# Optimization experiments

Hardware: AMD Instinct MI355X
Metric: run time of the kernel (lower is better)

Reference implementation:

```python
import jax, jax.numpy as jnp
import numpy as np

B, T, IN, H, BN, OUT = 512, 257, 32, 128, 256, 64
K_SUB = 4  # RK4 substeps per knot interval (fixed-step stand-in for adaptive cdeint)


def setup_inputs() -> dict:
    key = jax.random.key(0)
    ks = jax.random.split(key, 12)

    def gl(k, shape):
        fan_in = shape[0]
        return (jax.random.normal(k, shape, jnp.float32) / np.sqrt(fan_in)).astype(jnp.float32)

    t = jnp.arange(T, dtype=jnp.float32) * 0.05  # sorted time knots, t[0]=t0
    z0 = jax.random.normal(ks[0], (B, H), jnp.float32)
    # control path: smooth-ish random walk sampled at the knots
    X = jnp.cumsum(jax.random.normal(ks[1], (B, T, IN), jnp.float32) * 0.1, axis=1)
    return {
        "t": t, "z0": z0, "X": X,
        "W1": gl(ks[2], (H, BN)), "b1": jnp.zeros((BN,), jnp.float32),
        "W2": gl(ks[3], (BN, BN)), "b2": jnp.zeros((BN,), jnp.float32),
        "W3": gl(ks[4], (BN, IN * H)), "b3": jnp.zeros((IN * H,), jnp.float32),
        "mW": gl(ks[5], (H, OUT)), "mb": jnp.zeros((OUT,), jnp.float32),
        "sW": gl(ks[6], (H, OUT)), "sb": jnp.zeros((OUT,), jnp.float32),
    }


def reference(t, z0, X, W1, b1, W2, b2, W3, b3, mW, mb, sW, sb):
    def cde_func(z):  # z: [B,H] -> [B,H,IN]
        h = jax.nn.relu(z @ W1 + b1)
        h = jax.nn.relu(h @ W2 + b2)
        o = jnp.tanh(h @ W3 + b3)
        return o.reshape(z.shape[0], H, IN)

    def vf(z, dxdt):  # dz/dt = f(z) @ dX/dt
        return jnp.einsum('bhi,bi->bh', cde_func(z), dxdt)

    dt_int = t[1:] - t[:-1]                       # [T-1]
    dXdt = (X[:, 1:] - X[:, :-1]) / dt_int[None, :, None]  # [B,T-1,IN], const per interval

    def interval_step(z, inp):
        dxdt, dti = inp
        hstep = dti / K_SUB
        def sub(zc, _):
            k1 = vf(zc, dxdt)
            k2 = vf(zc + 0.5 * hstep * k1, dxdt)
            k3 = vf(zc + 0.5 * hstep * k2, dxdt)
            k4 = vf(zc + hstep * k3, dxdt)
            zn = zc + (hstep / 6.0) * (k1 + 2.0 * k2 + 2.0 * k3 + k4)
            return zn, None
        z, _ = jax.lax.scan(sub, z, None, length=K_SUB)
        return z, z

    _, zs = jax.lax.scan(interval_step, z0, (jnp.moveaxis(dXdt, 1, 0), dt_int))
    zs = jnp.moveaxis(zs, 0, 1)  # z at t[1:] -> [B, T-1, H] (matches [1:].permute(1,0,2))

    mean_pred = zs @ mW + mb
    std_pred = jax.nn.softplus(zs @ sW + sb)
    return mean_pred, std_pred
```

## Files before the change

kernel.cpp:

```cpp
#include <hip/hip_runtime.h>


using short8   = __attribute__((ext_vector_type(8))) short;
using float4v  = __attribute__((ext_vector_type(4))) float;

__device__ unsigned short g_w1p[32768];
__device__ unsigned short g_w2p[65536];
__device__ unsigned short g_w3p[1048576];
__device__ unsigned short g_mwp[8192];
__device__ unsigned short g_swp[8192];

__device__ int   g_flag[256];
__device__ float g_zx[2 * 64 * 4 * 256];

__global__ void reset_flags(){
  if (threadIdx.x < 256) g_flag[threadIdx.x] = -1;
}

__device__ __forceinline__ unsigned short* pack_dst(int which){
  switch (which){
    case 0:  return g_w1p;
    case 1:  return g_w2p;
    case 2:  return g_w3p;
    case 3:  return g_mwp;
    default: return g_swp;
  }
}

__device__ __forceinline__ float bf2f(unsigned short h){
  union { unsigned int u; float f; } v; v.u = ((unsigned int)h) << 16; return v.f;
}
__device__ __forceinline__ unsigned short f2bf(float f){
  union { float f; unsigned int u; } v; v.f = f;
  unsigned int u = v.u;
  return (unsigned short)((u + 0x7FFFu + ((u >> 16) & 1u)) >> 16);
}
template<bool BF16> __device__ __forceinline__ float loadf(const void* p, long i){
  if constexpr (BF16) return bf2f(((const unsigned short*)p)[i]);
  else                return ((const float*)p)[i];
}
__device__ __forceinline__ bool input_is_bf16(const void* t){
  return ((const unsigned short*)t)[1] != 0;
}
__device__ __forceinline__ float tanh_f(float x){
  float e = __builtin_amdgcn_exp2f(x * 2.88539008177793f);
  return 1.f - 2.f * __builtin_amdgcn_rcpf(e + 1.f);
}
__device__ __forceinline__ float softplus_f(float x){
  if (x > 20.f) return x;
  float e = __builtin_amdgcn_exp2f(x * 1.44269504088896f);
  return __builtin_amdgcn_logf(1.f + e) * 0.693147180559945f;
}
__device__ __forceinline__ float row_sum16(float v){
  int x;
  x = __builtin_amdgcn_update_dpp(0, __float_as_int(v), 0x118, 0xF, 0xF, true);
  v += __int_as_float(x);
  x = __builtin_amdgcn_update_dpp(0, __float_as_int(v), 0x114, 0xF, 0xF, true);
  v += __int_as_float(x);
  x = __builtin_amdgcn_update_dpp(0, __float_as_int(v), 0x112, 0xF, 0xF, true);
  v += __int_as_float(x);
  x = __builtin_amdgcn_update_dpp(0, __float_as_int(v), 0x111, 0xF, 0xF, true);
  v += __int_as_float(x);
  return v;
}

template<bool BF16>
__global__ __launch_bounds__(256)
void pack_weight(const void* __restrict__ src, int which,
                 int K, int N, const void* __restrict__ tchk){
  if (input_is_bf16(tchk) != BF16) return;
  unsigned short* dst = pack_dst(which);
  const int KT = K >> 5;
  const long total = (long)(N >> 4) * KT * 512;
  for (long e = (long)blockIdx.x * blockDim.x + threadIdx.x; e < total;
       e += (long)gridDim.x * blockDim.x){
    int  r    = (int)(e & 511);
    long tile = e >> 9;
    int  kt   = (int)(tile % KT);
    int  nt   = (int)(tile / KT);
    int  ln   = r >> 3, j = r & 7;
    int  k    = (kt << 5) + ((ln >> 4) << 3) + j;
    int  n    = (nt << 4) + (ln & 15);
    long si   = (long)k * N + n;
    dst[e] = BF16 ? ((const unsigned short*)src)[si] : f2bf(((const float*)src)[si]);
  }
}

#define STRZ 136
#define STRH 264
#define STRV 36
#define STRD 33
#define W3C_NT 16

template<bool BF16>
__global__ __launch_bounds__(1024, 4)
void cde_main(const void* __restrict__ tin,  const void* __restrict__ z0in,
              const void* __restrict__ Xin,
              const void* __restrict__ b1in, const void* __restrict__ b2in,
              const void* __restrict__ b3in, const void* __restrict__ mbin,
              const void* __restrict__ sbin,
              void* __restrict__ outv)
{
  if (input_is_bf16(tin) != BF16) return;

  const unsigned short* __restrict__ w1p = g_w1p;
  const unsigned short* __restrict__ w2p = g_w2p;
  const unsigned short* __restrict__ w3p = g_w3p;
  const unsigned short* __restrict__ mwp = g_mwp;
  const unsigned short* __restrict__ swp = g_swp;

  __shared__ __align__(16) unsigned short bufZ [16 * STRZ];
  __shared__ __align__(16) unsigned short bufH1[16 * STRH];
  __shared__ __align__(16) unsigned short bufH2[16 * STRH];
  __shared__ __align__(16) float          vfs  [ 8 * STRV];
  __shared__ __align__(16) float          dxs  [ 8 * STRD];
  __shared__ __align__(16) float          biasl[1664];
  __shared__ __align__(16) unsigned short w3c  [W3C_NT * 4096];

  const int tid  = threadIdx.x;
  const int lane = tid & 63;
  const int wv   = tid >> 6;
  const int c16  = lane & 15;
  const int quad = lane >> 4;
  const int hq   = blockIdx.x & 3;
  const int grp  = blockIdx.x >> 2;
  const int m0   = grp * 8;

  for (int i = tid; i < 1664; i += 1024){
    float v;
    if      (i < 256)  v = loadf<BF16>(b1in, i);
    else if (i < 512)  v = loadf<BF16>(b2in, i - 256);
    else if (i < 1536) v = loadf<BF16>(b3in, hq * 1024 + (i - 512));
    else if (i < 1600) v = loadf<BF16>(mbin, i - 1536);
    else               v = loadf<BF16>(sbin, i - 1600);
    biasl[i] = v;
  }

  for (int e = tid * 8; e < W3C_NT * 4096; e += 1024 * 8){
    const int s = e >> 12;
    const int o = e & 4095;
    *(short8*)&w3c[e] =
      *(const short8*)&w3p[(((long)(hq * 512 + s * 32)) << 9) + o];
  }

  short8 w1f[4], w2f[8];
  {
    const unsigned short* p1 = w1p + ((long)(wv * 4) << 9) + lane * 8;
    #pragma unroll
    for (int kt = 0; kt < 4; ++kt) w1f[kt] = *(const short8*)(p1 + (kt << 9));
    const unsigned short* p2 = w2p + ((long)(wv * 8) << 9) + lane * 8;
    #pragma unroll
    for (int kt = 0; kt < 8; ++kt) w2f[kt] = *(const short8*)(p2 + (kt << 9));
    #pragma unroll
    for (int kt = 0; kt < 4; ++kt) asm volatile("" : "+v"(w1f[kt]));
    #pragma unroll
    for (int kt = 0; kt < 8; ++kt) asm volatile("" : "+v"(w2f[kt]));
  }

  const int  zm   = tid >> 7;
  const int  zd   = tid & 127;
  const bool own  = (zd >> 5) == hq;
  const int  xidx = zm * 32 + (zd & 31);
  float z = loadf<BF16>(z0in, (long)(m0 + zm) * 128 + zd);
  float zacc = 0.f;
  {
    unsigned short h = f2bf(z);
    bufZ[(2 * zm    ) * STRZ + zd] = h;
    bufZ[(2 * zm + 1) * STRZ + zd] = f2bf(z - bf2f(h));
  }

  for (int ti = 0; ti < 256; ++ti){
    const float dt = loadf<BF16>(tin, ti + 1) - loadf<BF16>(tin, ti);
    const float hs = dt * 0.25f;
    if (tid < 256){
      const int m = tid >> 5, i = tid & 31;
      float xc = loadf<BF16>(Xin, ((long)(m0 + m) * 257 + ti    ) * 32 + i);
      float xn = loadf<BF16>(Xin, ((long)(m0 + m) * 257 + ti + 1) * 32 + i);
      dxs[m * STRD + i] = (xn - xc) / dt;
    }
    __syncthreads();
    float dd[2][2];
    #pragma unroll
    for (int ih = 0; ih < 2; ++ih)
      #pragma unroll
      for (int s = 0; s < 2; ++s)
        dd[ih][s] = dxs[(quad * 2 + s) * STRD + ih * 16 + c16];

    for (int sub = 0; sub < 4; ++sub){
      for (int st = 0; st < 4; ++st){
        const int stg = (ti << 4) + (sub << 2) + st;
        const int par = stg & 1;
        __syncthreads();

        {
          short8 a[4];
          #pragma unroll
          for (int kt = 0; kt < 4; ++kt)
            a[kt] = *(const short8*)&bufZ[c16 * STRZ + kt * 32 + quad * 8];
          float4v acc = { 0.f, 0.f, 0.f, 0.f };
          #pragma unroll
          for (int kt = 0; kt < 4; ++kt)
            acc = __builtin_amdgcn_mfma_f32_16x16x32_bf16(a[kt], w1f[kt], acc, 0, 0, 0);
          const float bv = biasl[wv * 16 + c16];
          #pragma unroll
          for (int s = 0; s < 2; ++s){
            float v = acc[2 * s] + acc[2 * s + 1] + bv;
            v = v > 0.f ? v : 0.f;
            unsigned short h = f2bf(v);
            const int row = quad * 4 + 2 * s;
            bufH1[ row      * STRH + wv * 16 + c16] = h;
            bufH1[(row + 1) * STRH + wv * 16 + c16] = f2bf(v - bf2f(h));
          }
        }
        __syncthreads();

        {
          short8 a[8];
          #pragma unroll
          for (int kt = 0; kt < 8; ++kt)
            a[kt] = *(const short8*)&bufH1[c16 * STRH + kt * 32 + quad * 8];
          float4v acc = { 0.f, 0.f, 0.f, 0.f };
          #pragma unroll
          for (int kt = 0; kt < 8; ++kt)
            acc = __builtin_amdgcn_mfma_f32_16x16x32_bf16(a[kt], w2f[kt], acc, 0, 0, 0);
          const float bv = biasl[256 + wv * 16 + c16];
          #pragma unroll
          for (int s = 0; s < 2; ++s){
            float v = acc[2 * s] + acc[2 * s + 1] + bv;
            v = v > 0.f ? v : 0.f;
            unsigned short h = f2bf(v);
            const int row = quad * 4 + 2 * s;
            bufH2[ row      * STRH + wv * 16 + c16] = h;
            bufH2[(row + 1) * STRH + wv * 16 + c16] = f2bf(v - bf2f(h));
          }
        }
        __syncthreads();

        {
          short8 a[8];
          #pragma unroll
          for (int kt = 0; kt < 8; ++kt)
            a[kt] = *(const short8*)&bufH2[c16 * STRH + kt * 32 + quad * 8];

          #pragma unroll 1
          for (int j = 0; j < 4; j += 2){
            const int lnt = wv * 4 + j;
            float t0[2], t1[2];
            {
              float4v acc = { 0.f, 0.f, 0.f, 0.f };
              if (j == 0){
                const unsigned short* cp = &w3c[wv * 4096] + lane * 8;
                #pragma unroll
                for (int kh = 0; kh < 2; ++kh){
                  short8 b[4];
                  #pragma unroll
                  for (int kt = 0; kt < 4; ++kt)
                    b[kt] = *(const short8*)(cp + ((kh * 4 + kt) << 9));
                  #pragma unroll
                  for (int kt = 0; kt < 4; ++kt)
                    acc = __builtin_amdgcn_mfma_f32_16x16x32_bf16(a[kh * 4 + kt], b[kt], acc, 0, 0, 0);
                }
              } else {
                const unsigned short* wp = w3p + (((long)(hq * 512 + lnt * 8)) << 9) + lane * 8;
                #pragma unroll
                for (int kh = 0; kh < 2; ++kh){
                  short8 b[4];
                  #pragma unroll
                  for (int kt = 0; kt < 4; ++kt)
                    b[kt] = *(const short8*)(wp + ((kh * 4 + kt) << 9));
                  #pragma unroll
                  for (int kt = 0; kt < 4; ++kt)
                    acc = __builtin_amdgcn_mfma_f32_16x16x32_bf16(a[kh * 4 + kt], b[kt], acc, 0, 0, 0);
                }
              }
              const float bv = biasl[512 + lnt * 16 + c16];
              #pragma unroll
              for (int s = 0; s < 2; ++s)
                t0[s] = tanh_f(acc[2 * s] + acc[2 * s + 1] + bv) * dd[0][s];
            }
            {
              const int nt = lnt + 1;
              float4v acc = { 0.f, 0.f, 0.f, 0.f };
              {
                const unsigned short* wp = w3p + (((long)(hq * 512 + nt * 8)) << 9) + lane * 8;
                #pragma unroll
                for (int kh = 0; kh < 2; ++kh){
                  short8 b[4];
                  #pragma unroll
                  for (int kt = 0; kt < 4; ++kt)
                    b[kt] = *(const short8*)(wp + ((kh * 4 + kt) << 9));
                  #pragma unroll
                  for (int kt = 0; kt < 4; ++kt)
                    acc = __builtin_amdgcn_mfma_f32_16x16x32_bf16(a[kh * 4 + kt], b[kt], acc, 0, 0, 0);
                }
              }
              const float bv = biasl[512 + nt * 16 + c16];
              #pragma unroll
              for (int s = 0; s < 2; ++s)
                t1[s] = tanh_f(acc[2 * s] + acc[2 * s + 1] + bv) * dd[1][s];
              const int hl = lnt >> 1;
              #pragma unroll
              for (int s = 0; s < 2; ++s){
                float r = row_sum16(t0[s] + t1[s]);
                if (c16 == 15) vfs[(quad * 2 + s) * STRV + hl] = r;
              }
            }
          }
        }
        __syncthreads();

        if (own){
          const float k = vfs[zm * STRV + (zd & 31)];
          float nin;
          if (st == 0){
            zacc = z + (hs * (1.f / 6.f)) * k;
            nin  = z + 0.5f * hs * k;
          } else if (st == 1){
            zacc += (hs * (1.f / 3.f)) * k;
            nin   = z + 0.5f * hs * k;
          } else if (st == 2){
            zacc += (hs * (1.f / 3.f)) * k;
            nin   = z + hs * k;
          } else {
            z    = zacc + (hs * (1.f / 6.f)) * k;
            nin  = z;
          }
          __hip_atomic_store((int*)&g_zx[((par * 64 + grp) * 4 + hq) * 256 + xidx],
                             __float_as_int(nin),
                             __ATOMIC_RELAXED, __HIP_MEMORY_SCOPE_AGENT);
          unsigned short h = f2bf(nin);
          bufZ[(2 * zm    ) * STRZ + zd] = h;
          bufZ[(2 * zm + 1) * STRZ + zd] = f2bf(nin - bf2f(h));
        }
        __syncthreads();
        if (tid == 0)
          __hip_atomic_store(&g_flag[blockIdx.x], stg,
                             __ATOMIC_RELAXED, __HIP_MEMORY_SCOPE_AGENT);
        if (tid < 3){
          const int p = (grp << 2) | ((hq + 1 + tid) & 3);
          while (__hip_atomic_load(&g_flag[p],
                                   __ATOMIC_RELAXED, __HIP_MEMORY_SCOPE_AGENT) < stg)
            __builtin_amdgcn_s_sleep(2);
        }
        __syncthreads();
        if (!own){
          const int q = zd >> 5;
          int u = __hip_atomic_load(
                    (const int*)&g_zx[((par * 64 + grp) * 4 + q) * 256 + xidx],
                    __ATOMIC_RELAXED, __HIP_MEMORY_SCOPE_AGENT);
          float v = __int_as_float(u);
          unsigned short h = f2bf(v);
          bufZ[(2 * zm    ) * STRZ + zd] = h;
          bufZ[(2 * zm + 1) * STRZ + zd] = f2bf(v - bf2f(h));
        }
      }
    }

    __syncthreads();
    if (hq < 2 && wv < 4){
      short8 a[4];
      #pragma unroll
      for (int kt = 0; kt < 4; ++kt)
        a[kt] = *(const short8*)&bufZ[c16 * STRZ + kt * 32 + quad * 8];
      const int  nt    = wv;
      const bool isStd = (hq == 1);
      const unsigned short* wp = (isStd ? swp : mwp) + ((long)(nt * 4) << 9) + lane * 8;
      short8 b[4];
      #pragma unroll
      for (int kt = 0; kt < 4; ++kt) b[kt] = *(const short8*)(wp + (kt << 9));
      float4v acc = { 0.f, 0.f, 0.f, 0.f };
      #pragma unroll
      for (int kt = 0; kt < 4; ++kt)
        acc = __builtin_amdgcn_mfma_f32_16x16x32_bf16(a[kt], b[kt], acc, 0, 0, 0);
      const float bv    = biasl[(isStd ? 1600 : 1536) + nt * 16 + c16];
      const long  obase = isStd ? 8388608L : 0L;
      #pragma unroll
      for (int s = 0; s < 2; ++s){
        float v = acc[2 * s] + acc[2 * s + 1] + bv;
        if (isStd) v = softplus_f(v);
        long oi = obase + ((long)(m0 + quad * 2 + s) * 256 + ti) * 64 + nt * 16 + c16;
        if constexpr (BF16) ((unsigned short*)outv)[oi] = f2bf(v);
        else                ((float*)outv)[oi] = v;
      }
    }
  }
}

extern "C" void kernel_launch(void* const* d_in, const int* in_sizes, int n_in,
                              void* d_out, int out_size, void* d_ws, size_t ws_size,
                              hipStream_t stream)
{
  const void* t  = d_in[0];
  const void* z0 = d_in[1];
  const void* X  = d_in[2];
  const void* W1 = d_in[3];
  const void* b1 = d_in[4];
  const void* W2 = d_in[5];
  const void* b2 = d_in[6];
  const void* W3 = d_in[7];
  const void* b3 = d_in[8];
  const void* mW = d_in[9];
  const void* mb = d_in[10];
  const void* sW = d_in[11];
  const void* sb = d_in[12];

  pack_weight<true ><<<256, 256, 0, stream>>>(W1, 0, 128,  256, t);
  pack_weight<true ><<<256, 256, 0, stream>>>(W2, 1, 256,  256, t);
  pack_weight<true ><<<512, 256, 0, stream>>>(W3, 2, 256, 4096, t);
  pack_weight<true ><<< 64, 256, 0, stream>>>(mW, 3, 128,   64, t);
  pack_weight<true ><<< 64, 256, 0, stream>>>(sW, 4, 128,   64, t);
  pack_weight<false><<<256, 256, 0, stream>>>(W1, 0, 128,  256, t);
  pack_weight<false><<<256, 256, 0, stream>>>(W2, 1, 256,  256, t);
  pack_weight<false><<<512, 256, 0, stream>>>(W3, 2, 256, 4096, t);
  pack_weight<false><<< 64, 256, 0, stream>>>(mW, 3, 128,   64, t);
  pack_weight<false><<< 64, 256, 0, stream>>>(sW, 4, 128,   64, t);

  reset_flags<<<1, 256, 0, stream>>>();

  cde_main<true ><<<256, 1024, 0, stream>>>(t, z0, X, b1, b2, b3, mb, sb, d_out);
  cde_main<false><<<256, 1024, 0, stream>>>(t, z0, X, b1, b2, b3, mb, sb, d_out);
  (void)in_sizes; (void)n_in; (void)out_size; (void)d_ws; (void)ws_size;
}
```

Before: 28.76 ms.

## Repartition blocks to 16 batch rows × 8 hidden slices with shared W3 fragments

Each block now handles 16 batch rows (two MFMA halves) and one eighth of the hidden dimension instead of 8 rows and one quarter, so 8 cooperating blocks exchange z through global memory per group. W3 fragments are loaded once per wave and reused across both row halves, which doubles reuse of the large W3 stream and halves the number of W3 columns per block. The cost is more cross-block synchronization partners (7 flags polled instead of 3), more exchanged z values, and a smaller LDS cache of W3 (13 tiles), with the rest read from global memory each stage.

```diff
diff --git a/kernel.cpp b/kernel.cpp
--- a/kernel.cpp
+++ b/kernel.cpp
@@ -11,7 +11,7 @@
 __device__ unsigned short g_swp[8192];
 
 __device__ int   g_flag[256];
-__device__ float g_zx[2 * 64 * 4 * 256];
+__device__ float g_zx[2 * 32 * 8 * 256];
 
 __global__ void reset_flags(){
   if (threadIdx.x < 256) g_flag[threadIdx.x] = -1;
@@ -88,9 +88,9 @@
 
 #define STRZ 136
 #define STRH 264
-#define STRV 36
+#define STRVW 20
 #define STRD 33
-#define W3C_NT 16
+#define W3C_NT 13
 
 template<bool BF16>
 __global__ __launch_bounds__(1024, 4)
@@ -109,12 +109,12 @@
   const unsigned short* __restrict__ mwp = g_mwp;
   const unsigned short* __restrict__ swp = g_swp;
 
-  __shared__ __align__(16) unsigned short bufZ [16 * STRZ];
-  __shared__ __align__(16) unsigned short bufH1[16 * STRH];
-  __shared__ __align__(16) unsigned short bufH2[16 * STRH];
-  __shared__ __align__(16) float          vfs  [ 8 * STRV];
-  __shared__ __align__(16) float          dxs  [ 8 * STRD];
-  __shared__ __align__(16) float          biasl[1664];
+  __shared__ __align__(16) unsigned short bufZ [32 * STRZ];
+  __shared__ __align__(16) unsigned short bufH1[32 * STRH];
+  __shared__ __align__(16) unsigned short bufH2[32 * STRH];
+  __shared__ __align__(16) float          vfs  [16 * STRVW];
+  __shared__ __align__(16) float          dxs  [16 * STRD];
+  __shared__ __align__(16) float          biasl[1152];
   __shared__ __align__(16) unsigned short w3c  [W3C_NT * 4096];
 
   const int tid  = threadIdx.x;
@@ -122,17 +122,17 @@
   const int wv   = tid >> 6;
   const int c16  = lane & 15;
   const int quad = lane >> 4;
-  const int hq   = blockIdx.x & 3;
-  const int grp  = blockIdx.x >> 2;
-  const int m0   = grp * 8;
-
-  for (int i = tid; i < 1664; i += 1024){
+  const int ho   = blockIdx.x & 7;
+  const int grp  = blockIdx.x >> 3;
+  const int m0   = grp * 16;
+
+  for (int i = tid; i < 1152; i += 1024){
     float v;
     if      (i < 256)  v = loadf<BF16>(b1in, i);
     else if (i < 512)  v = loadf<BF16>(b2in, i - 256);
-    else if (i < 1536) v = loadf<BF16>(b3in, hq * 1024 + (i - 512));
-    else if (i < 1600) v = loadf<BF16>(mbin, i - 1536);
-    else               v = loadf<BF16>(sbin, i - 1600);
+    else if (i < 1024) v = loadf<BF16>(b3in, ho * 512 + (i - 512));
+    else if (i < 1088) v = loadf<BF16>(mbin, i - 1024);
+    else               v = loadf<BF16>(sbin, i - 1088);
     biasl[i] = v;
   }
 
@@ -140,7 +140,7 @@
     const int s = e >> 12;
     const int o = e & 4095;
     *(short8*)&w3c[e] =
-      *(const short8*)&w3p[(((long)(hq * 512 + s * 32)) << 9) + o];
+      *(const short8*)&w3p[((long)(ho * 32 + 2 * s)) * 4096 + o];
   }
 
   short8 w1f[4], w2f[8];
@@ -151,40 +151,44 @@
     const unsigned short* p2 = w2p + ((long)(wv * 8) << 9) + lane * 8;
     #pragma unroll
     for (int kt = 0; kt < 8; ++kt) w2f[kt] = *(const short8*)(p2 + (kt << 9));
-    #pragma unroll
-    for (int kt = 0; kt < 4; ++kt) asm volatile("" : "+v"(w1f[kt]));
-    #pragma unroll
-    for (int kt = 0; kt < 8; ++kt) asm volatile("" : "+v"(w2f[kt]));
   }
 
   const int  zm   = tid >> 7;
   const int  zd   = tid & 127;
-  const bool own  = (zd >> 5) == hq;
-  const int  xidx = zm * 32 + (zd & 31);
-  float z = loadf<BF16>(z0in, (long)(m0 + zm) * 128 + zd);
-  float zacc = 0.f;
+  const int  q    = zd >> 4;
+  const bool own  = (q == ho);
+  const int  d16  = zd & 15;
+  float z0r = loadf<BF16>(z0in, (long)(m0 + zm    ) * 128 + zd);
+  float z1r = loadf<BF16>(z0in, (long)(m0 + zm + 8) * 128 + zd);
+  float zacc0 = 0.f, zacc1 = 0.f;
   {
-    unsigned short h = f2bf(z);
-    bufZ[(2 * zm    ) * STRZ + zd] = h;
-    bufZ[(2 * zm + 1) * STRZ + zd] = f2bf(z - bf2f(h));
+    unsigned short h;
+    h = f2bf(z0r);
+    bufZ[( 2 * zm    ) * STRZ + zd] = h;
+    bufZ[( 2 * zm + 1) * STRZ + zd] = f2bf(z0r - bf2f(h));
+    h = f2bf(z1r);
+    bufZ[(16 + 2 * zm    ) * STRZ + zd] = h;
+    bufZ[(16 + 2 * zm + 1) * STRZ + zd] = f2bf(z1r - bf2f(h));
   }
 
   for (int ti = 0; ti < 256; ++ti){
     const float dt = loadf<BF16>(tin, ti + 1) - loadf<BF16>(tin, ti);
     const float hs = dt * 0.25f;
-    if (tid < 256){
+    if (tid < 512){
       const int m = tid >> 5, i = tid & 31;
       float xc = loadf<BF16>(Xin, ((long)(m0 + m) * 257 + ti    ) * 32 + i);
       float xn = loadf<BF16>(Xin, ((long)(m0 + m) * 257 + ti + 1) * 32 + i);
       dxs[m * STRD + i] = (xn - xc) / dt;
     }
     __syncthreads();
-    float dd[2][2];
+    float ddA[2][2], ddB[2][2];
     #pragma unroll
-    for (int ih = 0; ih < 2; ++ih)
+    for (int half = 0; half < 2; ++half)
       #pragma unroll
-      for (int s = 0; s < 2; ++s)
-        dd[ih][s] = dxs[(quad * 2 + s) * STRD + ih * 16 + c16];
+      for (int s = 0; s < 2; ++s){
+        ddA[half][s] = dxs[(half * 8 + quad * 2 + s) * STRD +      c16];
+        ddB[half][s] = dxs[(half * 8 + quad * 2 + s) * STRD + 16 + c16];
+      }
 
     for (int sub = 0; sub < 4; ++sub){
       for (int st = 0; st < 4; ++st){
@@ -193,177 +197,188 @@
         __syncthreads();
 
         {
-          short8 a[4];
-          #pragma unroll
-          for (int kt = 0; kt < 4; ++kt)
-            a[kt] = *(const short8*)&bufZ[c16 * STRZ + kt * 32 + quad * 8];
-          float4v acc = { 0.f, 0.f, 0.f, 0.f };
-          #pragma unroll
-          for (int kt = 0; kt < 4; ++kt)
-            acc = __builtin_amdgcn_mfma_f32_16x16x32_bf16(a[kt], w1f[kt], acc, 0, 0, 0);
           const float bv = biasl[wv * 16 + c16];
           #pragma unroll
-          for (int s = 0; s < 2; ++s){
-            float v = acc[2 * s] + acc[2 * s + 1] + bv;
-            v = v > 0.f ? v : 0.f;
-            unsigned short h = f2bf(v);
-            const int row = quad * 4 + 2 * s;
-            bufH1[ row      * STRH + wv * 16 + c16] = h;
-            bufH1[(row + 1) * STRH + wv * 16 + c16] = f2bf(v - bf2f(h));
+          for (int half = 0; half < 2; ++half){
+            short8 a[4];
+            #pragma unroll
+            for (int kt = 0; kt < 4; ++kt)
+              a[kt] = *(const short8*)&bufZ[(half * 16 + c16) * STRZ + kt * 32 + quad * 8];
+            float4v acc = { 0.f, 0.f, 0.f, 0.f };
+            #pragma unroll
+            for (int kt = 0; kt < 4; ++kt)
+              acc = __builtin_amdgcn_mfma_f32_16x16x32_bf16(a[kt], w1f[kt], acc, 0, 0, 0);
+            #pragma unroll
+            for (int s = 0; s < 2; ++s){
+              float v = acc[2 * s] + acc[2 * s + 1] + bv;
+              v = v > 0.f ? v : 0.f;
+              unsigned short h = f2bf(v);
+              const int row = half * 16 + quad * 4 + 2 * s;
+              bufH1[ row      * STRH + wv * 16 + c16] = h;
+              bufH1[(row + 1) * STRH + wv * 16 + c16] = f2bf(v - bf2f(h));
+            }
           }
         }
         __syncthreads();
 
         {
-          short8 a[8];
-          #pragma unroll
-          for (int kt = 0; kt < 8; ++kt)
-            a[kt] = *(const short8*)&bufH1[c16 * STRH + kt * 32 + quad * 8];
-          float4v acc = { 0.f, 0.f, 0.f, 0.f };
-          #pragma unroll
-          for (int kt = 0; kt < 8; ++kt)
-            acc = __builtin_amdgcn_mfma_f32_16x16x32_bf16(a[kt], w2f[kt], acc, 0, 0, 0);
           const float bv = biasl[256 + wv * 16 + c16];
           #pragma unroll
-          for (int s = 0; s < 2; ++s){
-            float v = acc[2 * s] + acc[2 * s + 1] + bv;
-            v = v > 0.f ? v : 0.f;
-            unsigned short h = f2bf(v);
-            const int row = quad * 4 + 2 * s;
-            bufH2[ row      * STRH + wv * 16 + c16] = h;
-            bufH2[(row + 1) * STRH + wv * 16 + c16] = f2bf(v - bf2f(h));
+          for (int half = 0; half < 2; ++half){
+            short8 a[8];
+            #pragma unroll
+            for (int kt = 0; kt < 8; ++kt)
+              a[kt] = *(const short8*)&bufH1[(half * 16 + c16) * STRH + kt * 32 + quad * 8];
+            float4v acc = { 0.f, 0.f, 0.f, 0.f };
+            #pragma unroll
+            for (int kt = 0; kt < 8; ++kt)
+              acc = __builtin_amdgcn_mfma_f32_16x16x32_bf16(a[kt], w2f[kt], acc, 0, 0, 0);
+            #pragma unroll
+            for (int s = 0; s < 2; ++s){
+              float v = acc[2 * s] + acc[2 * s + 1] + bv;
+              v = v > 0.f ? v : 0.f;
+              unsigned short h = f2bf(v);
+              const int row = half * 16 + quad * 4 + 2 * s;
+              bufH2[ row      * STRH + wv * 16 + c16] = h;
+              bufH2[(row + 1) * STRH + wv * 16 + c16] = f2bf(v - bf2f(h));
+            }
           }
         }
         __syncthreads();
 
         {
-          short8 a[8];
+          float t0[2][2], t1[2][2];
+          {
+            short8 b[8];
+            if (wv < W3C_NT){
+              const unsigned short* cp = &w3c[wv * 4096] + lane * 8;
+              #pragma unroll
+              for (int kt = 0; kt < 8; ++kt) b[kt] = *(const short8*)(cp + (kt << 9));
+            } else {
+              const unsigned short* wp = w3p + ((long)(ho * 32 + 2 * wv)) * 4096 + lane * 8;
+              #pragma unroll
+              for (int kt = 0; kt < 8; ++kt) b[kt] = *(const short8*)(wp + (kt << 9));
+            }
+            const float bv = biasl[512 + (2 * wv) * 16 + c16];
+            #pragma unroll
+            for (int half = 0; half < 2; ++half){
+              short8 a[8];
+              #pragma unroll
+              for (int kt = 0; kt < 8; ++kt)
+                a[kt] = *(const short8*)&bufH2[(half * 16 + c16) * STRH + kt * 32 + quad * 8];
+              float4v acc = { 0.f, 0.f, 0.f, 0.f };
+              #pragma unroll
+              for (int kt = 0; kt < 8; ++kt)
+                acc = __builtin_amdgcn_mfma_f32_16x16x32_bf16(a[kt], b[kt], acc, 0, 0, 0);
+              #pragma unroll
+              for (int s = 0; s < 2; ++s)
+                t0[half][s] = tanh_f(acc[2 * s] + acc[2 * s + 1] + bv) * ddA[half][s];
+            }
+          }
+          {
+            short8 b[8];
+            const unsigned short* wp = w3p + ((long)(ho * 32 + 2 * wv + 1)) * 4096 + lane * 8;
+            #pragma unroll
+            for (int kt = 0; kt < 8; ++kt) b[kt] = *(const short8*)(wp + (kt << 9));
+            const float bv = biasl[512 + (2 * wv + 1) * 16 + c16];
+            #pragma unroll
+            for (int half = 0; half < 2; ++half){
+              short8 a[8];
+              #pragma unroll
+              for (int kt = 0; kt < 8; ++kt)
+                a[kt] = *(const short8*)&bufH2[(half * 16 + c16) * STRH + kt * 32 + quad * 8];
+              float4v acc = { 0.f, 0.f, 0.f, 0.f };
+              #pragma unroll
+              for (int kt = 0; kt < 8; ++kt)
+                acc = __builtin_amdgcn_mfma_f32_16x16x32_bf16(a[kt], b[kt], acc, 0, 0, 0);
+              #pragma unroll
+              for (int s = 0; s < 2; ++s)
+                t1[half][s] = tanh_f(acc[2 * s] + acc[2 * s + 1] + bv) * ddB[half][s];
+            }
+          }
           #pragma unroll
-          for (int kt = 0; kt < 8; ++kt)
-            a[kt] = *(const short8*)&bufH2[c16 * STRH + kt * 32 + quad * 8];
-
-          #pragma unroll 1
-          for (int j = 0; j < 4; j += 2){
-            const int lnt = wv * 4 + j;
-            float t0[2], t1[2];
-            {
-              float4v acc = { 0.f, 0.f, 0.f, 0.f };
-              if (j == 0){
-                const unsigned short* cp = &w3c[wv * 4096] + lane * 8;
-                #pragma unroll
-                for (int kh = 0; kh < 2; ++kh){
-                  short8 b[4];
-                  #pragma unroll
-                  for (int kt = 0; kt < 4; ++kt)
-                    b[kt] = *(const short8*)(cp + ((kh * 4 + kt) << 9));
-                  #pragma unroll
-                  for (int kt = 0; kt < 4; ++kt)
-                    acc = __builtin_amdgcn_mfma_f32_16x16x32_bf16(a[kh * 4 + kt], b[kt], acc, 0, 0, 0);
-                }
-              } else {
-                const unsigned short* wp = w3p + (((long)(hq * 512 + lnt * 8)) << 9) + lane * 8;
-                #pragma unroll
-                for (int kh = 0; kh < 2; ++kh){
-                  short8 b[4];
-                  #pragma unroll
-                  for (int kt = 0; kt < 4; ++kt)
-                    b[kt] = *(const short8*)(wp + ((kh * 4 + kt) << 9));
-                  #pragma unroll
-                  for (int kt = 0; kt < 4; ++kt)
-                    acc = __builtin_amdgcn_mfma_f32_16x16x32_bf16(a[kh * 4 + kt], b[kt], acc, 0, 0, 0);
-                }
-              }
-              const float bv = biasl[512 + lnt * 16 + c16];
-              #pragma unroll
-              for (int s = 0; s < 2; ++s)
-                t0[s] = tanh_f(acc[2 * s] + acc[2 * s + 1] + bv) * dd[0][s];
-            }
-            {
-              const int nt = lnt + 1;
-              float4v acc = { 0.f, 0.f, 0.f, 0.f };
-              {
-                const unsigned short* wp = w3p + (((long)(hq * 512 + nt * 8)) << 9) + lane * 8;
-                #pragma unroll
-                for (int kh = 0; kh < 2; ++kh){
-                  short8 b[4];
-                  #pragma unroll
-                  for (int kt = 0; kt < 4; ++kt)
-                    b[kt] = *(const short8*)(wp + ((kh * 4 + kt) << 9));
-                  #pragma unroll
-                  for (int kt = 0; kt < 4; ++kt)
-                    acc = __builtin_amdgcn_mfma_f32_16x16x32_bf16(a[kh * 4 + kt], b[kt], acc, 0, 0, 0);
-                }
-              }
-              const float bv = biasl[512 + nt * 16 + c16];
-              #pragma unroll
-              for (int s = 0; s < 2; ++s)
-                t1[s] = tanh_f(acc[2 * s] + acc[2 * s + 1] + bv) * dd[1][s];
-              const int hl = lnt >> 1;
-              #pragma unroll
-              for (int s = 0; s < 2; ++s){
-                float r = row_sum16(t0[s] + t1[s]);
-                if (c16 == 15) vfs[(quad * 2 + s) * STRV + hl] = r;
-              }
-            }
-          }
+          for (int half = 0; half < 2; ++half)
+            #pragma unroll
+            for (int s = 0; s < 2; ++s){
+              float r = row_sum16(t0[half][s] + t1[half][s]);
+              if (c16 == 15) vfs[(half * 8 + quad * 2 + s) * STRVW + wv] = r;
+            }
         }
         __syncthreads();
 
         if (own){
-          const float k = vfs[zm * STRV + (zd & 31)];
-          float nin;
-          if (st == 0){
-            zacc = z + (hs * (1.f / 6.f)) * k;
-            nin  = z + 0.5f * hs * k;
-          } else if (st == 1){
-            zacc += (hs * (1.f / 3.f)) * k;
-            nin   = z + 0.5f * hs * k;
-          } else if (st == 2){
-            zacc += (hs * (1.f / 3.f)) * k;
-            nin   = z + hs * k;
-          } else {
-            z    = zacc + (hs * (1.f / 6.f)) * k;
-            nin  = z;
-          }
-          __hip_atomic_store((int*)&g_zx[((par * 64 + grp) * 4 + hq) * 256 + xidx],
-                             __float_as_int(nin),
-                             __ATOMIC_RELAXED, __HIP_MEMORY_SCOPE_AGENT);
-          unsigned short h = f2bf(nin);
-          bufZ[(2 * zm    ) * STRZ + zd] = h;
-          bufZ[(2 * zm + 1) * STRZ + zd] = f2bf(nin - bf2f(h));
+          {
+            const float k = vfs[zm * STRVW + d16];
+            float nin;
+            if (st == 0){ zacc0 = z0r + (hs * (1.f/6.f)) * k; nin = z0r + 0.5f*hs*k; }
+            else if (st == 1){ zacc0 += (hs * (1.f/3.f)) * k; nin = z0r + 0.5f*hs*k; }
+            else if (st == 2){ zacc0 += (hs * (1.f/3.f)) * k; nin = z0r + hs*k; }
+            else { z0r = zacc0 + (hs * (1.f/6.f)) * k; nin = z0r; }
+            __hip_atomic_store((int*)&g_zx[((par * 32 + grp) * 8 + ho) * 256 + zm * 16 + d16],
+                               __float_as_int(nin),
+                               __ATOMIC_RELAXED, __HIP_MEMORY_SCOPE_AGENT);
+            unsigned short h = f2bf(nin);
+            bufZ[(2 * zm    ) * STRZ + zd] = h;
+            bufZ[(2 * zm + 1) * STRZ + zd] = f2bf(nin - bf2f(h));
+          }
+          {
+            const float k = vfs[(zm + 8) * STRVW + d16];
+            float nin;
+            if (st == 0){ zacc1 = z1r + (hs * (1.f/6.f)) * k; nin = z1r + 0.5f*hs*k; }
+            else if (st == 1){ zacc1 += (hs * (1.f/3.f)) * k; nin = z1r + 0.5f*hs*k; }
+            else if (st == 2){ zacc1 += (hs * (1.f/3.f)) * k; nin = z1r + hs*k; }
+            else { z1r = zacc1 + (hs * (1.f/6.f)) * k; nin = z1r; }
+            __hip_atomic_store((int*)&g_zx[((par * 32 + grp) * 8 + ho) * 256 + (zm + 8) * 16 + d16],
+                               __float_as_int(nin),
+                               __ATOMIC_RELAXED, __HIP_MEMORY_SCOPE_AGENT);
+            unsigned short h = f2bf(nin);
+            bufZ[(16 + 2 * zm    ) * STRZ + zd] = h;
+            bufZ[(16 + 2 * zm + 1) * STRZ + zd] = f2bf(nin - bf2f(h));
+          }
         }
         __syncthreads();
         if (tid == 0)
           __hip_atomic_store(&g_flag[blockIdx.x], stg,
                              __ATOMIC_RELAXED, __HIP_MEMORY_SCOPE_AGENT);
-        if (tid < 3){
-          const int p = (grp << 2) | ((hq + 1 + tid) & 3);
+        if (tid >= 1 && tid < 8){
+          const int p = (grp << 3) | ((ho + tid) & 7);
           while (__hip_atomic_load(&g_flag[p],
                                    __ATOMIC_RELAXED, __HIP_MEMORY_SCOPE_AGENT) < stg)
             __builtin_amdgcn_s_sleep(2);
         }
         __syncthreads();
         if (!own){
-          const int q = zd >> 5;
-          int u = __hip_atomic_load(
-                    (const int*)&g_zx[((par * 64 + grp) * 4 + q) * 256 + xidx],
-                    __ATOMIC_RELAXED, __HIP_MEMORY_SCOPE_AGENT);
-          float v = __int_as_float(u);
-          unsigned short h = f2bf(v);
-          bufZ[(2 * zm    ) * STRZ + zd] = h;
-          bufZ[(2 * zm + 1) * STRZ + zd] = f2bf(v - bf2f(h));
+          {
+            int u = __hip_atomic_load(
+                      (const int*)&g_zx[((par * 32 + grp) * 8 + q) * 256 + zm * 16 + d16],
+                      __ATOMIC_RELAXED, __HIP_MEMORY_SCOPE_AGENT);
+            float v = __int_as_float(u);
+            unsigned short h = f2bf(v);
+            bufZ[(2 * zm    ) * STRZ + zd] = h;
+            bufZ[(2 * zm + 1) * STRZ + zd] = f2bf(v - bf2f(h));
+          }
+          {
+            int u = __hip_atomic_load(
+                      (const int*)&g_zx[((par * 32 + grp) * 8 + q) * 256 + (zm + 8) * 16 + d16],
+                      __ATOMIC_RELAXED, __HIP_MEMORY_SCOPE_AGENT);
+            float v = __int_as_float(u);
+            unsigned short h = f2bf(v);
+            bufZ[(16 + 2 * zm    ) * STRZ + zd] = h;
+            bufZ[(16 + 2 * zm + 1) * STRZ + zd] = f2bf(v - bf2f(h));
+          }
         }
       }
     }
 
     __syncthreads();
-    if (hq < 2 && wv < 4){
+    if (ho < 2 && wv < 8){
+      const int  half  = wv >> 2;
+      const int  nt    = wv & 3;
+      const bool isStd = (ho == 1);
       short8 a[4];
       #pragma unroll
       for (int kt = 0; kt < 4; ++kt)
-        a[kt] = *(const short8*)&bufZ[c16 * STRZ + kt * 32 + quad * 8];
-      const int  nt    = wv;
-      const bool isStd = (hq == 1);
+        a[kt] = *(const short8*)&bufZ[(half * 16 + c16) * STRZ + kt * 32 + quad * 8];
       const unsigned short* wp = (isStd ? swp : mwp) + ((long)(nt * 4) << 9) + lane * 8;
       short8 b[4];
       #pragma unroll
@@ -372,13 +387,14 @@
       #pragma unroll
       for (int kt = 0; kt < 4; ++kt)
         acc = __builtin_amdgcn_mfma_f32_16x16x32_bf16(a[kt], b[kt], acc, 0, 0, 0);
-      const float bv    = biasl[(isStd ? 1600 : 1536) + nt * 16 + c16];
+      const float bv    = biasl[(isStd ? 1088 : 1024) + nt * 16 + c16];
       const long  obase = isStd ? 8388608L : 0L;
       #pragma unroll
       for (int s = 0; s < 2; ++s){
         float v = acc[2 * s] + acc[2 * s + 1] + bv;
         if (isStd) v = softplus_f(v);
-        long oi = obase + ((long)(m0 + quad * 2 + s) * 256 + ti) * 64 + nt * 16 + c16;
+        long oi = obase + ((long)(m0 + half * 8 + quad * 2 + s) * 256 + ti) * 64
+                        + nt * 16 + c16;
         if constexpr (BF16) ((unsigned short*)outv)[oi] = f2bf(v);
         else                ((float*)outv)[oi] = v;
       }
```

After: 65.64 ms. 2.28x slower.
